# Optimization experiments

Measured on AMD Instinct MI355X. Metric: run time of the kernel, lower is better.

The kernel has to match this reference:

```python
import jax, jax.numpy as jnp
import numpy as np

B, S, D_IN, D_OUT = 4, 2048, 1024, 1024

def setup_inputs() -> dict:
    key = jax.random.key(0)
    kx, kq, kk, kv = jax.random.split(key, 4)
    x = jax.random.normal(kx, (B, S, D_IN), dtype=jnp.float32)
    scale = 1.0 / np.sqrt(D_IN)
    Wq = jax.random.normal(kq, (D_IN, D_OUT), dtype=jnp.float32) * scale
    Wk = jax.random.normal(kk, (D_IN, D_OUT), dtype=jnp.float32) * scale
    Wv = jax.random.normal(kv, (D_IN, D_OUT), dtype=jnp.float32) * scale
    return {"x": x, "Wq": Wq, "Wk": Wk, "Wv": Wv}

def reference(x, Wq, Wk, Wv):
    # x: [B, S, d_in]; Linear without bias -> x @ W
    q = jnp.einsum('bsd,de->bse', x, Wq)
    k = jnp.einsum('bsd,de->bse', x, Wk)
    v = jnp.einsum('bsd,de->bse', x, Wv)
    S_len = x.shape[1]
    scores = jnp.einsum('bqe,bke->bqk', q, k)  # [B, S, S]
    causal = jnp.triu(jnp.ones((S_len, S_len), dtype=bool), k=1)
    scores = jnp.where(causal[None, :, :], -jnp.inf, scores)
    inv_sqrt_d = jnp.asarray(1.0 / np.sqrt(k.shape[-1]), dtype=scores.dtype)
    weights = jax.nn.softmax(scores * inv_sqrt_d, axis=-1)
    # dropout=0.0 -> identity
    return jnp.einsum('bqk,bke->bqe', weights, v)
```

## Files before the change

### kernel.cpp

```cpp
#include <hip/hip_runtime.h>
#include <cstdint>

#define DEV __device__ __forceinline__

typedef unsigned short u16;
typedef unsigned int   u32;
typedef __bf16 bf16x8 __attribute__((ext_vector_type(8)));
typedef float  f32x4  __attribute__((ext_vector_type(4)));

static constexpr int BATCH = 4;
static constexpr int SEQ   = 2048;
static constexpr int DMODEL= 1024;
static constexpr int MPROJ = BATCH * SEQ;

DEV u16 f2bf(float f) {
    u32 u = __float_as_uint(f);
    u32 r = (u + 0x7FFFu + ((u >> 16) & 1u)) >> 16;
    return (u16)r;
}
DEV float bf2f(u16 u) { return __uint_as_float(((u32)u) << 16); }

DEV void async16(const void* g, void* l) {
    __builtin_amdgcn_global_load_lds(
        (__attribute__((address_space(1))) void*)(g),
        (__attribute__((address_space(3))) void*)(l),
        16, 0, 0);
}

__global__ void conv_x_kernel(const float* __restrict__ x, u16* __restrict__ xb, int n8) {
    int i = blockIdx.x * blockDim.x + threadIdx.x;
    if (i >= n8) return;
    const float4* p = (const float4*)x + (size_t)i * 2;
    float4 a = p[0], b = p[1];
    uint4 o;
    o.x = (u32)f2bf(a.x) | ((u32)f2bf(a.y) << 16);
    o.y = (u32)f2bf(a.z) | ((u32)f2bf(a.w) << 16);
    o.z = (u32)f2bf(b.x) | ((u32)f2bf(b.y) << 16);
    o.w = (u32)f2bf(b.z) | ((u32)f2bf(b.w) << 16);
    ((uint4*)xb)[i] = o;
}

__global__ void convW_kernel(const float* __restrict__ Wq, const float* __restrict__ Wk,
                             const float* __restrict__ Wv, u16* __restrict__ Wt) {
    __shared__ u16 tile[32][33];
    int z = blockIdx.z;
    const float* src = (z == 0) ? Wq : (z == 1 ? Wk : Wv);
    u16* dst = Wt + (size_t)z * DMODEL * DMODEL;
    int k0 = blockIdx.x * 32, n0 = blockIdx.y * 32;
    int tx = threadIdx.x, ty = threadIdx.y;
    #pragma unroll
    for (int j = 0; j < 4; ++j)
        tile[ty + j * 8][tx] = f2bf(src[(size_t)(k0 + ty + j * 8) * DMODEL + n0 + tx]);
    __syncthreads();
    #pragma unroll
    for (int j = 0; j < 4; ++j)
        dst[(size_t)(n0 + ty + j * 8) * DMODEL + k0 + tx] = tile[tx][ty + j * 8];
}

__global__ void transV_kernel(const u16* __restrict__ V, u16* __restrict__ Vt) {
    __shared__ u16 tile[32][33];
    int b = blockIdx.z;
    int s0 = blockIdx.x * 32, d0 = blockIdx.y * 32;
    const u16* src = V + (size_t)b * SEQ * DMODEL;
    u16* dst = Vt + (size_t)b * DMODEL * SEQ;
    int tx = threadIdx.x, ty = threadIdx.y;
    #pragma unroll
    for (int j = 0; j < 4; ++j)
        tile[ty + j * 8][tx] = src[(size_t)(s0 + ty + j * 8) * DMODEL + d0 + tx];
    __syncthreads();
    #pragma unroll
    for (int j = 0; j < 4; ++j)
        dst[(size_t)(d0 + ty + j * 8) * SEQ + s0 + tx] = tile[tx][ty + j * 8];
}

template <int EPI, bool TRI, bool CK>
__global__ __launch_bounds__(256)
void gemm_bt(const u16* __restrict__ A, const u16* __restrict__ Bt, void* __restrict__ Cv,
             int N, int K, int NB, long sA, long sB, long sC, float scale,
             float* __restrict__ lsum) {
    __shared__ __bf16 lsA[128 * 32];
    __shared__ __bf16 lsB[128 * 32];

    int bx = blockIdx.x, b = blockIdx.y;
    { int q = (int)(gridDim.x >> 3); bx = (bx & 7) * q + (bx >> 3); }
    int mb, nb;
    if (TRI) {
        int t = bx;
        int r = (int)((sqrtf(8.f * (float)t + 1.f) - 1.f) * 0.5f);
        while ((r + 1) * (r + 2) / 2 <= t) ++r;
        while (r * (r + 1) / 2 > t) --r;
        mb = r; nb = t - r * (r + 1) / 2;
    } else {
        mb = bx / NB; nb = bx % NB;
    }
    const u16* Ab = A + (size_t)b * sA;
    const u16* Bb = Bt + (size_t)b * sB;

    const int m0 = mb * 128, n0 = nb * 128;
    const int keff = CK ? min(K, (mb + 1) * 128) : K;

    const int tid = threadIdx.x, wid = tid >> 6, lane = tid & 63;
    const int wm = (wid >> 1) * 64, wn = (wid & 1) * 64;

    const char* gA = (const char*)(Ab + (size_t)(m0 + wid * 32 + (lane >> 2)) * K) + (lane & 3) * 16;
    const char* gB = (const char*)(Bb + (size_t)(n0 + wid * 32 + (lane >> 2)) * K) + (lane & 3) * 16;
    const long rowskip = (long)16 * K * 2;
    __bf16* lA0 = &lsA[wid * 1024];
    __bf16* lB0 = &lsB[wid * 1024];

    f32x4 zero = {0.f, 0.f, 0.f, 0.f};
    f32x4 acc[4][4];
    #pragma unroll
    for (int i = 0; i < 4; ++i)
        #pragma unroll
        for (int j = 0; j < 4; ++j) acc[i][j] = zero;

    const int aoff = (wm + (lane & 15)) * 32 + (lane >> 4) * 8;
    const int boff = (wn + (lane & 15)) * 32 + (lane >> 4) * 8;

    const int nkt = keff >> 5;
    for (int kt = 0; kt < nkt; ++kt) {
        __syncthreads();
        async16(gA, lA0);            async16(gA + rowskip, lA0 + 512);
        async16(gB, lB0);            async16(gB + rowskip, lB0 + 512);
        gA += 64; gB += 64;
        __syncthreads();

        bf16x8 af[4], bf[4];
        #pragma unroll
        for (int i = 0; i < 4; ++i)
            af[i] = *reinterpret_cast<const bf16x8*>(&lsA[aoff + i * 512]);
        #pragma unroll
        for (int i = 0; i < 4; ++i)
            bf[i] = *reinterpret_cast<const bf16x8*>(&lsB[boff + i * 512]);

        #pragma unroll
        for (int mi = 0; mi < 4; ++mi)
            #pragma unroll
            for (int ni = 0; ni < 4; ++ni)
                acc[mi][ni] = __builtin_amdgcn_mfma_f32_16x16x32_bf16(
                    af[mi], bf[ni], acc[mi][ni], 0, 0, 0);
    }

    const int crow0 = m0 + wm + ((lane >> 4) << 2);
    const int ccol0 = n0 + wn + (lane & 15);

    if constexpr (EPI == 0) {
        u16* Cb = (u16*)Cv + (size_t)b * sC;
        #pragma unroll
        for (int mi = 0; mi < 4; ++mi)
            #pragma unroll
            for (int ni = 0; ni < 4; ++ni)
                #pragma unroll
                for (int j = 0; j < 4; ++j)
                    Cb[(size_t)(crow0 + mi * 16 + j) * N + (ccol0 + ni * 16)] =
                        f2bf(acc[mi][ni][j] * scale);
    } else if constexpr (EPI == 1) {
        u16* Cb = (u16*)Cv + (size_t)b * sC;
        float* lb = lsum + (size_t)b * SEQ;
        #pragma unroll
        for (int mi = 0; mi < 4; ++mi)
            #pragma unroll
            for (int j = 0; j < 4; ++j) {
                const int crow = crow0 + mi * 16 + j;
                float rsum = 0.f;
                #pragma unroll
                for (int ni = 0; ni < 4; ++ni) {
                    const int ccol = ccol0 + ni * 16;
                    float e = (ccol <= crow) ? __expf(acc[mi][ni][j] * scale) : 0.f;
                    rsum += e;
                    Cb[(size_t)crow * N + ccol] = f2bf(e);
                }
                rsum += __shfl_xor(rsum, 1);
                rsum += __shfl_xor(rsum, 2);
                rsum += __shfl_xor(rsum, 4);
                rsum += __shfl_xor(rsum, 8);
                if ((lane & 15) == 0) atomicAdd(&lb[crow], rsum);
            }
    } else {
        float* Cb = (float*)Cv + (size_t)b * sC;
        const float* lb = lsum + (size_t)b * SEQ;
        #pragma unroll
        for (int mi = 0; mi < 4; ++mi)
            #pragma unroll
            for (int j = 0; j < 4; ++j) {
                const int crow = crow0 + mi * 16 + j;
                const float inv = 1.f / lb[crow];
                #pragma unroll
                for (int ni = 0; ni < 4; ++ni)
                    Cb[(size_t)crow * N + (ccol0 + ni * 16)] = acc[mi][ni][j] * inv;
            }
    }
}

extern "C" void kernel_launch(void* const* d_in, const int* in_sizes, int n_in,
                              void* d_out, int out_size, void* d_ws, size_t ws_size,
                              hipStream_t stream) {
    const float* x  = (const float*)d_in[0];
    const float* Wq = (const float*)d_in[1];
    const float* Wk = (const float*)d_in[2];
    const float* Wv = (const float*)d_in[3];
    float* out = (float*)d_out;

    char* w = (char*)d_ws;
    u16* xb = (u16*)(w);
    u16* Wt = (u16*)(w + (16L << 20));
    u16* Q  = (u16*)(w + (22L << 20));
    u16* Kb = (u16*)(w + (38L << 20));
    u16* V  = (u16*)(w + (54L << 20));
    u16* Vt = (u16*)(w + (70L << 20));
    u16* SP = (u16*)(w + (86L << 20));
    float* lsum = (float*)(w + (118L << 20));

    hipMemsetAsync(lsum, 0, (size_t)BATCH * SEQ * sizeof(float), stream);
    conv_x_kernel<<<(MPROJ * DMODEL / 8 + 255) / 256, 256, 0, stream>>>(x, xb, MPROJ * DMODEL / 8);
    convW_kernel<<<dim3(32, 32, 3), dim3(32, 8), 0, stream>>>(Wq, Wk, Wv, Wt);
    gemm_bt<0, false, false><<<dim3(512, 3), 256, 0, stream>>>(
        xb, Wt, Q, DMODEL, DMODEL, 8,
        0, (long)DMODEL * DMODEL, (long)MPROJ * DMODEL, 1.f, nullptr);
    transV_kernel<<<dim3(64, 32, 4), dim3(32, 8), 0, stream>>>(V, Vt);
    gemm_bt<1, true, false><<<dim3(136, 4), 256, 0, stream>>>(
        Q, Kb, SP, SEQ, DMODEL, 0,
        (long)SEQ * DMODEL, (long)SEQ * DMODEL, (long)SEQ * SEQ, 0.03125f, lsum);
    gemm_bt<2, false, true><<<dim3(128, 4), 256, 0, stream>>>(
        SP, Vt, out, DMODEL, SEQ, 8,
        (long)SEQ * SEQ, (long)DMODEL * SEQ, (long)SEQ * DMODEL, 1.f, lsum);
}
```

Before: 263.4 us.

## Double-buffer LDS with XOR swizzle and BK=64 for attention GEMMs

```diff
diff --git a/kernel.cpp b/kernel.cpp
--- a/kernel.cpp
+++ b/kernel.cpp
@@ -73,13 +73,82 @@
         dst[(size_t)(d0 + ty + j * 8) * SEQ + s0 + tx] = tile[tx][ty + j * 8];
 }
 
+__global__ __launch_bounds__(256)
+void gemm_bt(const u16* __restrict__ A, const u16* __restrict__ Bt, u16* __restrict__ C,
+             int N, int K, int NB, long sA, long sB, long sC) {
+    __shared__ __bf16 lsA[128 * 32];
+    __shared__ __bf16 lsB[128 * 32];
+
+    int bx = blockIdx.x, b = blockIdx.y;
+    { int q = (int)(gridDim.x >> 3); bx = (bx & 7) * q + (bx >> 3); }
+    int mb = bx / NB, nb = bx % NB;
+    const u16* Ab = A + (size_t)b * sA;
+    const u16* Bb = Bt + (size_t)b * sB;
+    u16* Cb = C + (size_t)b * sC;
+
+    const int m0 = mb * 128, n0 = nb * 128;
+    const int tid = threadIdx.x, wid = tid >> 6, lane = tid & 63;
+    const int wm = (wid >> 1) * 64, wn = (wid & 1) * 64;
+
+    const char* gA = (const char*)(Ab + (size_t)(m0 + wid * 32 + (lane >> 2)) * K) + (lane & 3) * 16;
+    const char* gB = (const char*)(Bb + (size_t)(n0 + wid * 32 + (lane >> 2)) * K) + (lane & 3) * 16;
+    const long rowskip = (long)16 * K * 2;
+    __bf16* lA0 = &lsA[wid * 1024];
+    __bf16* lB0 = &lsB[wid * 1024];
+
+    f32x4 zero = {0.f, 0.f, 0.f, 0.f};
+    f32x4 acc[4][4];
+    #pragma unroll
+    for (int i = 0; i < 4; ++i)
+        #pragma unroll
+        for (int j = 0; j < 4; ++j) acc[i][j] = zero;
+
+    const int aoff = (wm + (lane & 15)) * 32 + (lane >> 4) * 8;
+    const int boff = (wn + (lane & 15)) * 32 + (lane >> 4) * 8;
+
+    const int nkt = K >> 5;
+    for (int kt = 0; kt < nkt; ++kt) {
+        __syncthreads();
+        async16(gA, lA0);            async16(gA + rowskip, lA0 + 512);
+        async16(gB, lB0);            async16(gB + rowskip, lB0 + 512);
+        gA += 64; gB += 64;
+        __syncthreads();
+
+        bf16x8 af[4], bf[4];
+        #pragma unroll
+        for (int i = 0; i < 4; ++i)
+            af[i] = *reinterpret_cast<const bf16x8*>(&lsA[aoff + i * 512]);
+        #pragma unroll
+        for (int i = 0; i < 4; ++i)
+            bf[i] = *reinterpret_cast<const bf16x8*>(&lsB[boff + i * 512]);
+
+        #pragma unroll
+        for (int mi = 0; mi < 4; ++mi)
+            #pragma unroll
+            for (int ni = 0; ni < 4; ++ni)
+                acc[mi][ni] = __builtin_amdgcn_mfma_f32_16x16x32_bf16(
+                    af[mi], bf[ni], acc[mi][ni], 0, 0, 0);
+    }
+
+    const int crow0 = m0 + wm + ((lane >> 4) << 2);
+    const int ccol0 = n0 + wn + (lane & 15);
+    #pragma unroll
+    for (int mi = 0; mi < 4; ++mi)
+        #pragma unroll
+        for (int ni = 0; ni < 4; ++ni)
+            #pragma unroll
+            for (int j = 0; j < 4; ++j)
+                Cb[(size_t)(crow0 + mi * 16 + j) * N + (ccol0 + ni * 16)] =
+                    f2bf(acc[mi][ni][j]);
+}
+
 template <int EPI, bool TRI, bool CK>
 __global__ __launch_bounds__(256)
-void gemm_bt(const u16* __restrict__ A, const u16* __restrict__ Bt, void* __restrict__ Cv,
+void gemm_db(const u16* __restrict__ A, const u16* __restrict__ Bt, void* __restrict__ Cv,
              int N, int K, int NB, long sA, long sB, long sC, float scale,
              float* __restrict__ lsum) {
-    __shared__ __bf16 lsA[128 * 32];
-    __shared__ __bf16 lsB[128 * 32];
+    __shared__ __bf16 lsA[2][128 * 64];
+    __shared__ __bf16 lsB[2][128 * 64];
 
     int bx = blockIdx.x, b = blockIdx.y;
     { int q = (int)(gridDim.x >> 3); bx = (bx & 7) * q + (bx >> 3); }
@@ -102,11 +171,11 @@
     const int tid = threadIdx.x, wid = tid >> 6, lane = tid & 63;
     const int wm = (wid >> 1) * 64, wn = (wid & 1) * 64;
 
-    const char* gA = (const char*)(Ab + (size_t)(m0 + wid * 32 + (lane >> 2)) * K) + (lane & 3) * 16;
-    const char* gB = (const char*)(Bb + (size_t)(n0 + wid * 32 + (lane >> 2)) * K) + (lane & 3) * 16;
-    const long rowskip = (long)16 * K * 2;
-    __bf16* lA0 = &lsA[wid * 1024];
-    __bf16* lB0 = &lsB[wid * 1024];
+    const int srow = wid * 32 + (lane >> 3);
+    const int scol = (((lane & 7) ^ (lane >> 3)) << 4);
+    const char* gA = (const char*)(Ab + (size_t)(m0 + srow) * K) + scol;
+    const char* gB = (const char*)(Bb + (size_t)(n0 + srow) * K) + scol;
+    const long rowskip8 = (long)8 * K * 2;
 
     f32x4 zero = {0.f, 0.f, 0.f, 0.f};
     f32x4 acc[4][4];
@@ -115,47 +184,65 @@
         #pragma unroll
         for (int j = 0; j < 4; ++j) acc[i][j] = zero;
 
-    const int aoff = (wm + (lane & 15)) * 32 + (lane >> 4) * 8;
-    const int boff = (wn + (lane & 15)) * 32 + (lane >> 4) * 8;
-
-    const int nkt = keff >> 5;
+    const int arow = wm + (lane & 15);
+    const int brow = wn + (lane & 15);
+    const int swz  = (lane & 7) << 4;
+    const int cb0  = ((lane >> 4) << 4);
+
+#define STAGE_DB(kt, dd)                                                      \
+    {                                                                         \
+        const char* pa_ = gA + (size_t)(kt) * 128;                            \
+        const char* pb_ = gB + (size_t)(kt) * 128;                            \
+        _Pragma("unroll")                                                     \
+        for (int i_ = 0; i_ < 4; ++i_) {                                      \
+            async16(pa_ + i_ * rowskip8, &lsA[dd][(wid * 32 + i_ * 8) * 64]); \
+            async16(pb_ + i_ * rowskip8, &lsB[dd][(wid * 32 + i_ * 8) * 64]); \
+        }                                                                     \
+    }
+
+    const int nkt = keff >> 6;
+    STAGE_DB(0, 0);
+    __syncthreads();
+
+    int d = 0;
     for (int kt = 0; kt < nkt; ++kt) {
+        if (kt + 1 < nkt) STAGE_DB(kt + 1, d ^ 1);
+
+        const char* baseA = (const char*)lsA[d];
+        const char* baseB = (const char*)lsB[d];
+        bf16x8 af[2][4], bf[2][4];
+        #pragma unroll
+        for (int ks = 0; ks < 2; ++ks) {
+            const int cbs = (ks * 64 + cb0) ^ swz;
+            #pragma unroll
+            for (int mi = 0; mi < 4; ++mi)
+                af[ks][mi] = *(const bf16x8*)(baseA + (size_t)(arow + mi * 16) * 128 + cbs);
+            #pragma unroll
+            for (int ni = 0; ni < 4; ++ni)
+                bf[ks][ni] = *(const bf16x8*)(baseB + (size_t)(brow + ni * 16) * 128 + cbs);
+        }
+
+        __builtin_amdgcn_s_setprio(1);
+        #pragma unroll
+        for (int mi = 0; mi < 4; ++mi)
+            #pragma unroll
+            for (int ni = 0; ni < 4; ++ni) {
+                acc[mi][ni] = __builtin_amdgcn_mfma_f32_16x16x32_bf16(
+                    af[0][mi], bf[0][ni], acc[mi][ni], 0, 0, 0);
+                acc[mi][ni] = __builtin_amdgcn_mfma_f32_16x16x32_bf16(
+                    af[1][mi], bf[1][ni], acc[mi][ni], 0, 0, 0);
+            }
+        __builtin_amdgcn_s_setprio(0);
+
         __syncthreads();
-        async16(gA, lA0);            async16(gA + rowskip, lA0 + 512);
-        async16(gB, lB0);            async16(gB + rowskip, lB0 + 512);
-        gA += 64; gB += 64;
-        __syncthreads();
-
-        bf16x8 af[4], bf[4];
-        #pragma unroll
-        for (int i = 0; i < 4; ++i)
-            af[i] = *reinterpret_cast<const bf16x8*>(&lsA[aoff + i * 512]);
-        #pragma unroll
-        for (int i = 0; i < 4; ++i)
-            bf[i] = *reinterpret_cast<const bf16x8*>(&lsB[boff + i * 512]);
-
-        #pragma unroll
-        for (int mi = 0; mi < 4; ++mi)
-            #pragma unroll
-            for (int ni = 0; ni < 4; ++ni)
-                acc[mi][ni] = __builtin_amdgcn_mfma_f32_16x16x32_bf16(
-                    af[mi], bf[ni], acc[mi][ni], 0, 0, 0);
-    }
+        d ^= 1;
+    }
+#undef STAGE_DB
 
     const int crow0 = m0 + wm + ((lane >> 4) << 2);
     const int ccol0 = n0 + wn + (lane & 15);
 
-    if constexpr (EPI == 0) {
-        u16* Cb = (u16*)Cv + (size_t)b * sC;
-        #pragma unroll
-        for (int mi = 0; mi < 4; ++mi)
-            #pragma unroll
-            for (int ni = 0; ni < 4; ++ni)
-                #pragma unroll
-                for (int j = 0; j < 4; ++j)
-                    Cb[(size_t)(crow0 + mi * 16 + j) * N + (ccol0 + ni * 16)] =
-                        f2bf(acc[mi][ni][j] * scale);
-    } else if constexpr (EPI == 1) {
+    if constexpr (EPI == 1) {
         u16* Cb = (u16*)Cv + (size_t)b * sC;
         float* lb = lsum + (size_t)b * SEQ;
         #pragma unroll
@@ -215,14 +302,14 @@
     hipMemsetAsync(lsum, 0, (size_t)BATCH * SEQ * sizeof(float), stream);
     conv_x_kernel<<<(MPROJ * DMODEL / 8 + 255) / 256, 256, 0, stream>>>(x, xb, MPROJ * DMODEL / 8);
     convW_kernel<<<dim3(32, 32, 3), dim3(32, 8), 0, stream>>>(Wq, Wk, Wv, Wt);
-    gemm_bt<0, false, false><<<dim3(512, 3), 256, 0, stream>>>(
+    gemm_bt<<<dim3(512, 3), 256, 0, stream>>>(
         xb, Wt, Q, DMODEL, DMODEL, 8,
-        0, (long)DMODEL * DMODEL, (long)MPROJ * DMODEL, 1.f, nullptr);
+        0, (long)DMODEL * DMODEL, (long)MPROJ * DMODEL);
     transV_kernel<<<dim3(64, 32, 4), dim3(32, 8), 0, stream>>>(V, Vt);
-    gemm_bt<1, true, false><<<dim3(136, 4), 256, 0, stream>>>(
+    gemm_db<1, true, false><<<dim3(136, 4), 256, 0, stream>>>(
         Q, Kb, SP, SEQ, DMODEL, 0,
         (long)SEQ * DMODEL, (long)SEQ * DMODEL, (long)SEQ * SEQ, 0.03125f, lsum);
-    gemm_bt<2, false, true><<<dim3(128, 4), 256, 0, stream>>>(
+    gemm_db<2, false, true><<<dim3(128, 4), 256, 0, stream>>>(
         SP, Vt, out, DMODEL, SEQ, 8,
         (long)SEQ * SEQ, (long)DMODEL * SEQ, (long)SEQ * DMODEL, 1.f, lsum);
 }
```

Result: faster. 252.9 us (-4.0%).
